# Kernel optimization log

Hardware: AMD Instinct MI355X
Metric: run time of the kernel (lower is better)

Reference implementation:

```python
import jax, jax.numpy as jnp
from jax import lax
import numpy as np

B, IMG, PS = 64, 384, 16
DM, DS, DI = 96, 16, 96
DT_RANK = 6
NREP = 4
NCLS = 5
HP = IMG // PS            # 24 patches per side
N = HP * HP               # 576 tokens


def _ln(x, g, b):
    m = x.mean(-1, keepdims=True)
    v = ((x - m) ** 2).mean(-1, keepdims=True)
    return (x - m) * lax.rsqrt(v + 1e-5) * g + b


def setup_inputs() -> dict:
    key = jax.random.key(0)
    ks = jax.random.split(key, 16)
    nrm = lambda k, s: jax.random.normal(k, s, jnp.float32) * 0.02
    return {
        "x": jax.random.uniform(ks[0], (B, 3, IMG, IMG), jnp.float32),
        "W_pe": nrm(ks[1], (DM, 3, PS, PS)), "b_pe": jnp.zeros((DM,), jnp.float32),
        "W_vis": nrm(ks[2], (DM, 1)), "b_vis": jnp.zeros((1,), jnp.float32),
        "dn_g": jnp.ones((DM,), jnp.float32), "dn_b": jnp.zeros((DM,), jnp.float32),
        "W_gate": nrm(ks[3], (DM, DM)), "b_gate": jnp.zeros((DM,), jnp.float32),
        "ln_g": jnp.ones((DM,), jnp.float32), "ln_b": jnp.zeros((DM,), jnp.float32),
        "W_in": nrm(ks[4], (DM, 2 * DI)),
        "conv_w": nrm(ks[5], (DI, 1, 3)),
        "W_xproj": nrm(ks[6], (DI, DT_RANK + 2 * DS)),
        "W_dt": nrm(ks[7], (DT_RANK, DI)), "b_dt": jnp.full((DI,), -2.0, jnp.float32),
        "A_log": jnp.log(jnp.tile(jnp.arange(1, DS + 1, dtype=jnp.float32), (DI, 1))),
        "D": jnp.ones((DI,), jnp.float32),
        "W_out": nrm(ks[8], (DI, DM)),
        "hd_dw": nrm(ks[9], (DM, 1, 3, 3)),
        "bn_g": jnp.ones((DM,), jnp.float32), "bn_b": jnp.zeros((DM,), jnp.float32),
        "bn_m": jnp.zeros((DM,), jnp.float32), "bn_v": jnp.ones((DM,), jnp.float32),
        "W_heat": nrm(ks[10], (NCLS, DM)), "b_heat": jnp.full((NCLS,), -2.19, jnp.float32),
        "W_off": nrm(ks[11], (2, DM)), "b_off": jnp.zeros((2,), jnp.float32),
        "W_size": nrm(ks[12], (2, DM)), "b_size": jnp.zeros((2,), jnp.float32),
    }


def _forward(x, W_pe, b_pe, W_vis, b_vis, dn_g, dn_b, W_gate, b_gate,
             ln_g, ln_b, W_in, conv_w, W_xproj, W_dt, b_dt, A_log, D, W_out,
             hd_dw, bn_g, bn_b, bn_m, bn_v, W_heat, b_heat, W_off, b_off, W_size, b_size):
    # --- retinex preprocessing (single-scale, log domain) ---
    kblur = jnp.ones((3, 1, 5, 5), jnp.float32) / 25.0
    L = lax.conv_general_dilated(x, kblur, (1, 1), 'SAME',
                                 feature_group_count=3,
                                 dimension_numbers=('NCHW', 'OIHW', 'NCHW'))
    x = jnp.log1p(jnp.clip(x, 0.0)) - jnp.log1p(jnp.clip(L, 0.0))
    # --- patch embedding: strided conv -> tokens (B,N,DM) ---
    t = lax.conv_general_dilated(x, W_pe, (PS, PS), 'VALID',
                                 dimension_numbers=('NCHW', 'OIHW', 'NCHW'))
    t = t + b_pe[None, :, None, None]
    tokens = t.reshape(B, DM, N).transpose(0, 2, 1)
    # --- visibility estimator: per-token gate (B,N,1) ---
    vis = jax.nn.sigmoid(tokens @ W_vis + b_vis)
    # --- dual norm: LN + sigmoid gate ---
    tokens = _ln(tokens, dn_g, dn_b)
    norm_gate = jax.nn.sigmoid(tokens @ W_gate + b_gate)  # (B,N,DM)
    # --- weight-shared NC-SSM blocks ---
    A = -jnp.exp(A_log)  # (DI,DS)
    for _ in range(NREP):
        resid = tokens
        h = _ln(tokens, ln_g, ln_b)
        xz = h @ W_in                      # (B,N,2*DI)
        xin, z = xz[..., :DI], xz[..., DI:]
        # causal depthwise conv1d over sequence, kernel 3
        xc = xin.transpose(0, 2, 1)        # (B,DI,N)
        xc = lax.conv_general_dilated(xc, conv_w, (1,), [(2, 0)],
                                      feature_group_count=DI,
                                      dimension_numbers=('NCH', 'OIH', 'NCH'))
        xs = jax.nn.silu(xc.transpose(0, 2, 1))  # (B,N,DI)
        # selective-scan parameters
        proj = xs @ W_xproj                # (B,N,DT_RANK+2*DS)
        dt_raw = proj[..., :DT_RANK]
        Bc = proj[..., DT_RANK:DT_RANK + DS]
        Cc = proj[..., DT_RANK + DS:]
        dt = jax.nn.softplus(dt_raw @ W_dt + b_dt)  # (B,N,DI)
        # time-major scan
        def step(hst, inp):
            dt_t, B_t, C_t, x_t = inp      # (B,DI),(B,DS),(B,DS),(B,DI)
            dA = jnp.exp(dt_t[:, :, None] * A)                 # (B,DI,DS)
            hst = dA * hst + (dt_t * x_t)[:, :, None] * B_t[:, None, :]
            y = jnp.einsum('bds,bs->bd', hst, C_t)
            return hst, y
        h0 = jnp.zeros((B, DI, DS), jnp.float32)
        _, ys = lax.scan(step, h0, (dt.transpose(1, 0, 2), Bc.transpose(1, 0, 2),
                                    Cc.transpose(1, 0, 2), xs.transpose(1, 0, 2)))
        y = ys.transpose(1, 0, 2) + D * xs           # (B,N,DI)
        y = y * jax.nn.silu(z) * vis                  # gated by z and visibility
        tokens = resid + (y @ W_out) * norm_gate
    # --- CenterNet-style head ---
    f = tokens.transpose(0, 2, 1).reshape(B, DM, HP, HP)
    g = lax.conv_general_dilated(f, hd_dw, (1, 1), 'SAME',
                                 feature_group_count=DM,
                                 dimension_numbers=('NCHW', 'OIHW', 'NCHW'))
    g = (g - bn_m[None, :, None, None]) * lax.rsqrt(bn_v + 1e-5)[None, :, None, None]
    g = jax.nn.silu(g * bn_g[None, :, None, None] + bn_b[None, :, None, None])
    heat = jnp.einsum('bchw,oc->bohw', g, W_heat) + b_heat[None, :, None, None]
    off = jnp.einsum('bchw,oc->bohw', f, W_off) + b_off[None, :, None, None]
    size = jnp.einsum('bchw,oc->bohw', f, W_size) + b_size[None, :, None, None]
    return heat, off, size


def reference(x, W_pe, b_pe, W_vis, b_vis, dn_g, dn_b, W_gate, b_gate,
              ln_g, ln_b, W_in, conv_w, W_xproj, W_dt, b_dt, A_log, D, W_out,
              hd_dw, bn_g, bn_b, bn_m, bn_v, W_heat, b_heat, W_off, b_off, W_size, b_size):
    return _forward(x, W_pe, b_pe, W_vis, b_vis, dn_g, dn_b, W_gate, b_gate,
                    ln_g, ln_b, W_in, conv_w, W_xproj, W_dt, b_dt, A_log, D, W_out,
                    hd_dw, bn_g, bn_b, bn_m, bn_v, W_heat, b_heat, W_off, b_off,
                    W_size, b_size)
```

## Files before the change

### kernel.cpp

```cpp
#include <hip/hip_runtime.h>

#define DEVINL __device__ __forceinline__

typedef __attribute__((ext_vector_type(8))) short bf8v;
typedef __attribute__((ext_vector_type(4))) float f4v;

DEVINL float b2f(unsigned short u){ union{unsigned int i; float f;} x; x.i = ((unsigned int)u)<<16; return x.f; }
DEVINL unsigned short f2b(float f){ union{float f; unsigned int i;} x; x.f = f; unsigned int r = x.i + 0x7FFFu + ((x.i>>16)&1u); return (unsigned short)(r>>16); }
DEVINL float sigf(float v){ return 1.f/(1.f + __expf(-v)); }
DEVINL void unpack8(const uint4 u, float* d){
  d[0]=b2f((unsigned short)(u.x)); d[1]=b2f((unsigned short)(u.x>>16));
  d[2]=b2f((unsigned short)(u.y)); d[3]=b2f((unsigned short)(u.y>>16));
  d[4]=b2f((unsigned short)(u.z)); d[5]=b2f((unsigned short)(u.z>>16));
  d[6]=b2f((unsigned short)(u.w)); d[7]=b2f((unsigned short)(u.w>>16));
}
DEVINL uint4 pack8(const float* s){
  uint4 u;
  u.x = (unsigned int)f2b(s[0]) | ((unsigned int)f2b(s[1])<<16);
  u.y = (unsigned int)f2b(s[2]) | ((unsigned int)f2b(s[3])<<16);
  u.z = (unsigned int)f2b(s[4]) | ((unsigned int)f2b(s[5])<<16);
  u.w = (unsigned int)f2b(s[6]) | ((unsigned int)f2b(s[7])<<16);
  return u;
}
union FragU { uint4 u; bf8v v; };


#define PREP_STRIDE (128*256)
__global__ __launch_bounds__(256) void k_prep(
    const float* __restrict__ Wgate, const float* __restrict__ Win,
    const float* __restrict__ Wxproj, const float* __restrict__ Wdt,
    const float* __restrict__ Wout, const float* __restrict__ Alog,
    const float* __restrict__ Wpe, const float* __restrict__ convw,
    unsigned short* __restrict__ WgT, unsigned short* __restrict__ WiT,
    unsigned short* __restrict__ WxT, unsigned short* __restrict__ WoT,
    float* __restrict__ Amat, unsigned short* __restrict__ WpeB,
    float* __restrict__ cwsplit)
{
  int gtid = blockIdx.x*256 + threadIdx.x;
  for (int i = gtid; i < 9216; i += PREP_STRIDE){
    int n = i/96, k = i - n*96;
    WgT[n*96+k] = f2b(Wgate[k*96+n]);
    WoT[n*96+k] = f2b(Wout[k*96+n]);
  }
  for (int i = gtid; i < 18432; i += PREP_STRIDE){
    int n = i/96, k = i - n*96;
    WiT[n*96+k] = f2b(Win[k*192+n]);
  }
  for (int i = gtid; i < 12288; i += PREP_STRIDE){
    int n = i/96, k = i - n*96;
    if (n < 96){
      float s = 0.f;
      for (int r = 0; r < 6; ++r) s += Wxproj[k*38+r] * Wdt[r*96+n];
      WxT[n*96+k] = f2b(s);
    } else {
      WxT[n*96+k] = f2b(Wxproj[k*38 + 6 + (n-96)]);
    }
  }
  for (int i = gtid; i < 1536; i += PREP_STRIDE) Amat[i] = -__expf(Alog[i]);
  for (int i = gtid; i < 73728; i += PREP_STRIDE) WpeB[i] = f2b(Wpe[i]);
  for (int i = gtid; i < 96; i += PREP_STRIDE){
    cwsplit[i]       = convw[i*3+0];
    cwsplit[96+i]    = convw[i*3+1];
    cwsplit[192+i]   = convw[i*3+2];
  }
}

__global__ __launch_bounds__(256) void k_blur(const float* __restrict__ x,
                                              unsigned short* __restrict__ xlog)
{
  __shared__ float xt[12*384];
  __shared__ float vt[8*392];
  int bid = blockIdx.x;
  int tile = bid % 48; int bc = bid / 48; int c = bc % 3; int b = bc / 3;
  const float* xin = x + (size_t)(b*3 + c) * 147456;
  unsigned short* xout = xlog + (size_t)(b*3 + c) * 147456;
  int y0 = tile * 8;
  int tid = threadIdx.x;

  #pragma unroll
  for (int k = 0; k < 5; ++k){
    int idx = tid + k*256;
    if (idx < 1152){
      int r = idx / 96; int c4 = idx - r*96;
      int gy = y0 - 2 + r;
      float4 v = make_float4(0.f,0.f,0.f,0.f);
      if (gy >= 0 && gy < 384) v = *(const float4*)(xin + gy*384 + c4*4);
      *(float4*)(xt + r*384 + c4*4) = v;
    }
  }
  if (tid < 64){
    int r = tid >> 3; int j = tid & 7;
    vt[r*392 + ((j < 4) ? j : (384 + j))] = 0.f;
  }
  __syncthreads();

  #pragma unroll
  for (int k = 0; k < 2; ++k){
    int cc = tid + k*256;
    if (cc < 384){
      float x0 = xt[cc], x1 = xt[384+cc], x2 = xt[768+cc],
            x3 = xt[1152+cc], x4 = xt[1536+cc];
      float vs = ((x0+x1)+(x2+x3))+x4;
      vt[4+cc] = vs;
      #pragma unroll
      for (int r = 1; r < 8; ++r){
        vs += xt[(r+4)*384+cc] - xt[(r-1)*384+cc];
        vt[r*392+4+cc] = vs;
      }
    }
  }
  __syncthreads();

  #pragma unroll
  for (int k = 0; k < 3; ++k){
    int unit = tid + k*256;
    int r = unit / 96; int c4 = unit - r*96;
    int base = r*392 + 4 + c4*4;
    float f[12];
    *(float4*)(f)   = *(const float4*)(vt + base - 4);
    *(float4*)(f+4) = *(const float4*)(vt + base);
    *(float4*)(f+8) = *(const float4*)(vt + base + 4);
    float xv[4];
    *(float4*)(xv) = *(const float4*)(xt + (r+2)*384 + c4*4);
    ushort4 o;
    unsigned short* op = &o.x;
    #pragma unroll
    for (int j = 0; j < 4; ++j){
      float s = f[2+j] + f[3+j] + f[4+j] + f[5+j] + f[6+j];
      float L = fmaxf(s * 0.04f, 0.f);
      float xc = fmaxf(xv[j], 0.f);
      op[j] = f2b(__logf(1.f + xc) - __logf(1.f + L));
    }
    *(ushort4*)(xout + (y0+r)*384 + c4*4) = o;
  }
}

__global__ __launch_bounds__(256) void k_patchln(
    const unsigned short* __restrict__ xlog, const unsigned short* __restrict__ WpeB,
    const float* __restrict__ bpe, const float* __restrict__ dng,
    const float* __restrict__ dnb, const float* __restrict__ Wvis,
    const float* __restrict__ bvis, float* __restrict__ tok, float* __restrict__ vis)
{
  int wid = threadIdx.x >> 6, lane = threadIdx.x & 63;
  int m0 = (blockIdx.x*4 + wid)*16;
  int l15 = lane & 15, q = lane >> 4;
  int ma0 = m0 + l15;
  int b0 = ma0/576; int r0 = ma0 - b0*576; int hp0 = r0/24; int wp0 = r0 - hp0*24;
  size_t base0 = (size_t)b0*442368 + (size_t)hp0*6144 + (size_t)wp0*16;
  f4v acc[6];
  #pragma unroll
  for (int j=0;j<6;++j)
    #pragma unroll
    for (int r=0;r<4;++r) acc[j][r] = 0.f;
  for (int ks = 0; ks < 24; ++ks){
    int k0 = ks*32 + q*8;
    int c  = k0 >> 8;
    int ph = (k0 >> 4) & 15;
    int pw = k0 & 15;
    size_t off = (size_t)c*147456 + (size_t)ph*384 + pw;
    bf8v a0 = *(const bf8v*)(xlog + base0 + off);
    #pragma unroll
    for (int nf = 0; nf < 6; ++nf){
      bf8v bb = *(const bf8v*)(WpeB + (size_t)(nf*16 + l15)*768 + k0);
      acc[nf] = __builtin_amdgcn_mfma_f32_16x16x32_bf16(a0, bb, acc[nf], 0, 0, 0);
    }
  }
  float v[6][4];
  float s[4], w[4], vd[4];
  #pragma unroll
  for (int r=0;r<4;++r){ s[r]=0.f; w[r]=0.f; vd[r]=0.f; }
  #pragma unroll
  for (int nf=0; nf<6; ++nf){
    int n = nf*16 + l15;
    float bp = bpe[n];
    float wv = Wvis[n];
    #pragma unroll
    for (int r=0;r<4;++r){
      float t = acc[nf][r] + bp;
      v[nf][r] = t;
      s[r] += t; w[r] += t*t; vd[r] += t*wv;
    }
  }
  #pragma unroll
  for (int off=1; off<16; off<<=1){
    #pragma unroll
    for (int r=0;r<4;++r){
      s[r]  += __shfl_xor(s[r],  off);
      w[r]  += __shfl_xor(w[r],  off);
      vd[r] += __shfl_xor(vd[r], off);
    }
  }
  float mu[4], rs[4];
  #pragma unroll
  for (int r=0;r<4;++r){
    mu[r] = s[r]*(1.f/96.f);
    rs[r] = rsqrtf(fmaxf(w[r]*(1.f/96.f)-mu[r]*mu[r], 0.f) + 1e-5f);
  }
  if (l15 == 0){
    #pragma unroll
    for (int r=0;r<4;++r) vis[m0 + q*4 + r] = sigf(vd[r] + bvis[0]);
  }
  #pragma unroll
  for (int nf=0; nf<6; ++nf){
    int n = nf*16 + l15;
    float g = dng[n], bb = dnb[n];
    #pragma unroll
    for (int r=0;r<4;++r)
      tok[(size_t)(m0 + q*4 + r)*96 + n] = (v[nf][r]-mu[r])*rs[r]*g + bb;
  }
}

__global__ __launch_bounds__(256) void k_lnfull(const float* __restrict__ tokp,
    const unsigned short* __restrict__ WgT, const float* __restrict__ bg,
    const float* __restrict__ lng, const float* __restrict__ lnb,
    const unsigned short* __restrict__ WiT, const float* __restrict__ vis,
    unsigned short* __restrict__ gate, unsigned short* __restrict__ xin,
    unsigned short* __restrict__ zsv)
{
  int wid = threadIdx.x >> 6, lane = threadIdx.x & 63;
  int gid = blockIdx.x*4 + wid;
  int tile = gid >> 1, half = gid & 1;
  int m0 = tile*16;
  int l15 = lane & 15, q = lane >> 4;
  int ma0 = m0 + l15;
  float a0v[24];
  float s1=0.f, w1=0.f;
  bf8v fa[3];
  #pragma unroll
  for (int ks = 0; ks < 3; ++ks){
    int k0 = ks*32 + q*8;
    float v0[8];
    #pragma unroll
    for (int h = 0; h < 2; ++h){
      float4 va = *(const float4*)(tokp + (size_t)ma0*96 + k0 + h*4);
      int o = ks*8 + h*4;
      a0v[o+0]=va.x; a0v[o+1]=va.y; a0v[o+2]=va.z; a0v[o+3]=va.w;
      v0[h*4+0]=va.x; v0[h*4+1]=va.y; v0[h*4+2]=va.z; v0[h*4+3]=va.w;
      s1 += (va.x+va.y)+(va.z+va.w);
      w1 += (va.x*va.x+va.y*va.y)+(va.z*va.z+va.w*va.w);
    }
    FragU U0; U0.u = pack8(v0);
    fa[ks] = U0.v;
  }
  s1 += __shfl_xor(s1, 16); s1 += __shfl_xor(s1, 32);
  w1 += __shfl_xor(w1, 16); w1 += __shfl_xor(w1, 32);
  float mu1 = s1*(1.f/96.f);
  float rs1 = rsqrtf(fmaxf(w1*(1.f/96.f)-mu1*mu1, 0.f) + 1e-5f);
  bf8v fb[3];
  #pragma unroll
  for (int ks = 0; ks < 3; ++ks){
    int k0 = ks*32 + q*8;
    float gv[8], bv[8];
    *(float4*)(gv)   = *(const float4*)(lng + k0);
    *(float4*)(gv+4) = *(const float4*)(lng + k0 + 4);
    *(float4*)(bv)   = *(const float4*)(lnb + k0);
    *(float4*)(bv+4) = *(const float4*)(lnb + k0 + 4);
    float v0[8];
    #pragma unroll
    for (int j = 0; j < 8; ++j)
      v0[j] = (a0v[ks*8+j]-mu1)*rs1*gv[j] + bv[j];
    FragU U0; U0.u = pack8(v0);
    fb[ks] = U0.v;
  }
  {
    f4v ag[3];
    #pragma unroll
    for (int j=0;j<3;++j)
      #pragma unroll
      for (int r=0;r<4;++r) ag[j][r] = 0.f;
    const bf8v* bpg = (const bf8v*)(WgT) + (size_t)l15*12 + q;
    #pragma unroll
    for (int ks = 0; ks < 3; ++ks)
      #pragma unroll
      for (int nf = 0; nf < 3; ++nf){
        bf8v bb = bpg[(half*3+nf)*192 + ks*4];
        ag[nf] = __builtin_amdgcn_mfma_f32_16x16x32_bf16(fa[ks], bb, ag[nf], 0, 0, 0);
      }
    #pragma unroll
    for (int nf=0; nf<3; ++nf)
      #pragma unroll
      for (int r=0; r<4; ++r){
        int m = m0 + q*4 + r;
        int n = (half*3+nf)*16 + l15;
        gate[(size_t)m*96 + n] = f2b(sigf(ag[nf][r] + bg[n]));
      }
  }
  {
    f4v aw[6];
    #pragma unroll
    for (int j=0;j<6;++j)
      #pragma unroll
      for (int r=0;r<4;++r) aw[j][r] = 0.f;
    const bf8v* bpw = (const bf8v*)(WiT) + (size_t)l15*12 + q;
    #pragma unroll
    for (int ks = 0; ks < 3; ++ks)
      #pragma unroll
      for (int nf = 0; nf < 6; ++nf){
        bf8v bb = bpw[(half*6+nf)*192 + ks*4];
        aw[nf] = __builtin_amdgcn_mfma_f32_16x16x32_bf16(fb[ks], bb, aw[nf], 0, 0, 0);
      }
    if (half == 0){
      #pragma unroll
      for (int nf=0; nf<6; ++nf)
        #pragma unroll
        for (int r=0; r<4; ++r){
          int m = m0 + q*4 + r;
          int n = nf*16 + l15;
          xin[(size_t)m*96 + n] = f2b(aw[nf][r]);
        }
    } else {
      #pragma unroll
      for (int nf=0; nf<6; ++nf)
        #pragma unroll
        for (int r=0; r<4; ++r){
          int m = m0 + q*4 + r;
          int n = nf*16 + l15;
          float v = aw[nf][r];
          float sgl = v * sigf(v);
          zsv[(size_t)m*96 + n] = f2b(sgl * vis[m]);
        }
    }
  }
}

__global__ __launch_bounds__(256) void k_patchfull(
    const unsigned short* __restrict__ xlog, const unsigned short* __restrict__ WpeB,
    const float* __restrict__ bpe,
    const float* __restrict__ dng, const float* __restrict__ dnb,
    const float* __restrict__ Wvis, const float* __restrict__ bvis,
    const unsigned short* __restrict__ WgT, const float* __restrict__ bg,
    const float* __restrict__ lng, const float* __restrict__ lnb,
    const unsigned short* __restrict__ WiT,
    float* __restrict__ tok, unsigned short* __restrict__ gate,
    float* __restrict__ vis, unsigned short* __restrict__ xin,
    unsigned short* __restrict__ zsv)
{
  __shared__ float Sl[2][16][100];
  __shared__ float Vl[2][16];
  int wid = threadIdx.x >> 6, lane = threadIdx.x & 63;
  int gid = blockIdx.x*4 + wid;
  int tile = gid >> 1, half = gid & 1;
  int tl = wid >> 1;
  int m0 = tile*16;
  int l15 = lane & 15, q = lane >> 4;
  int ma0 = m0 + l15;

  {
    int b0 = ma0/576; int r0 = ma0 - b0*576; int hp0 = r0/24; int wp0 = r0 - hp0*24;
    size_t base0 = (size_t)b0*442368 + (size_t)hp0*6144 + (size_t)wp0*16;
    f4v acc[3];
    #pragma unroll
    for (int j=0;j<3;++j)
      #pragma unroll
      for (int r=0;r<4;++r) acc[j][r] = 0.f;
    for (int ks = 0; ks < 24; ++ks){
      int k0 = ks*32 + q*8;
      int c  = k0 >> 8;
      int ph = (k0 >> 4) & 15;
      int pw = k0 & 15;
      size_t off = (size_t)c*147456 + (size_t)ph*384 + pw;
      bf8v a0 = *(const bf8v*)(xlog + base0 + off);
      #pragma unroll
      for (int nf = 0; nf < 3; ++nf){
        bf8v bb = *(const bf8v*)(WpeB + (size_t)((half*3+nf)*16 + l15)*768 + k0);
        acc[nf] = __builtin_amdgcn_mfma_f32_16x16x32_bf16(a0, bb, acc[nf], 0, 0, 0);
      }
    }
    #pragma unroll
    for (int nf=0; nf<3; ++nf)
      #pragma unroll
      for (int r=0; r<4; ++r){
        int n = (half*3+nf)*16 + l15;
        Sl[tl][q*4+r][n] = acc[nf][r] + bpe[n];
      }
  }
  __syncthreads();

  float a0v[24];
  float s0=0.f, w0=0.f, vd=0.f;
  #pragma unroll
  for (int ks = 0; ks < 3; ++ks){
    int k0 = ks*32 + q*8;
    #pragma unroll
    for (int h = 0; h < 2; ++h){
      float4 va = *(const float4*)(&Sl[tl][l15][k0 + h*4]);
      float4 wv = *(const float4*)(Wvis + k0 + h*4);
      int o = ks*8 + h*4;
      a0v[o+0]=va.x; a0v[o+1]=va.y; a0v[o+2]=va.z; a0v[o+3]=va.w;
      s0 += (va.x+va.y)+(va.z+va.w);
      w0 += (va.x*va.x+va.y*va.y)+(va.z*va.z+va.w*va.w);
      vd += (va.x*wv.x+va.y*wv.y)+(va.z*wv.z+va.w*wv.w);
    }
  }
  s0 += __shfl_xor(s0, 16); s0 += __shfl_xor(s0, 32);
  w0 += __shfl_xor(w0, 16); w0 += __shfl_xor(w0, 32);
  vd += __shfl_xor(vd, 16); vd += __shfl_xor(vd, 32);
  float mu0 = s0*(1.f/96.f);
  float rs0 = rsqrtf(fmaxf(w0*(1.f/96.f)-mu0*mu0, 0.f) + 1e-5f);
  if (half == 0 && q == 0){
    float vv = sigf(vd + bvis[0]);
    vis[ma0] = vv;
    Vl[tl][l15] = vv;
  }

  bf8v fa[3];
  float s1=0.f, w1=0.f;
  #pragma unroll
  for (int ks = 0; ks < 3; ++ks){
    int k0 = ks*32 + q*8;
    float gv[8], bv[8];
    *(float4*)(gv)   = *(const float4*)(dng + k0);
    *(float4*)(gv+4) = *(const float4*)(dng + k0 + 4);
    *(float4*)(bv)   = *(const float4*)(dnb + k0);
    *(float4*)(bv+4) = *(const float4*)(dnb + k0 + 4);
    float v0[8];
    #pragma unroll
    for (int j = 0; j < 8; ++j){
      float v = (a0v[ks*8+j]-mu0)*rs0*gv[j] + bv[j];
      v0[j] = v;
      a0v[ks*8+j] = v;
      s1 += v; w1 += v*v;
    }
    if (half == 0){
      *(float4*)(tok + (size_t)ma0*96 + k0)     = make_float4(v0[0],v0[1],v0[2],v0[3]);
      *(float4*)(tok + (size_t)ma0*96 + k0 + 4) = make_float4(v0[4],v0[5],v0[6],v0[7]);
    }
    FragU U0; U0.u = pack8(v0);
    fa[ks] = U0.v;
  }

  {
    f4v ag[3];
    #pragma unroll
    for (int j=0;j<3;++j)
      #pragma unroll
      for (int r=0;r<4;++r) ag[j][r] = 0.f;
    const bf8v* bpg = (const bf8v*)(WgT) + (size_t)l15*12 + q;
    #pragma unroll
    for (int ks = 0; ks < 3; ++ks)
      #pragma unroll
      for (int nf = 0; nf < 3; ++nf){
        bf8v bb = bpg[(half*3+nf)*192 + ks*4];
        ag[nf] = __builtin_amdgcn_mfma_f32_16x16x32_bf16(fa[ks], bb, ag[nf], 0, 0, 0);
      }
    #pragma unroll
    for (int nf=0; nf<3; ++nf)
      #pragma unroll
      for (int r=0; r<4; ++r){
        int m = m0 + q*4 + r;
        int n = (half*3+nf)*16 + l15;
        gate[(size_t)m*96 + n] = f2b(sigf(ag[nf][r] + bg[n]));
      }
  }

  s1 += __shfl_xor(s1, 16); s1 += __shfl_xor(s1, 32);
  w1 += __shfl_xor(w1, 16); w1 += __shfl_xor(w1, 32);
  float mu1 = s1*(1.f/96.f);
  float rs1 = rsqrtf(fmaxf(w1*(1.f/96.f)-mu1*mu1, 0.f) + 1e-5f);
  bf8v fb[3];
  #pragma unroll
  for (int ks = 0; ks < 3; ++ks){
    int k0 = ks*32 + q*8;
    float gv[8], bv[8];
    *(float4*)(gv)   = *(const float4*)(lng + k0);
    *(float4*)(gv+4) = *(const float4*)(lng + k0 + 4);
    *(float4*)(bv)   = *(const float4*)(lnb + k0);
    *(float4*)(bv+4) = *(const float4*)(lnb + k0 + 4);
    float v0[8];
    #pragma unroll
    for (int j = 0; j < 8; ++j)
      v0[j] = (a0v[ks*8+j]-mu1)*rs1*gv[j] + bv[j];
    FragU U0; U0.u = pack8(v0);
    fb[ks] = U0.v;
  }
  __syncthreads();

  {
    f4v aw[6];
    #pragma unroll
    for (int j=0;j<6;++j)
      #pragma unroll
      for (int r=0;r<4;++r) aw[j][r] = 0.f;
    const bf8v* bpw = (const bf8v*)(WiT) + (size_t)l15*12 + q;
    #pragma unroll
    for (int ks = 0; ks < 3; ++ks)
      #pragma unroll
      for (int nf = 0; nf < 6; ++nf){
        bf8v bb = bpw[(half*6+nf)*192 + ks*4];
        aw[nf] = __builtin_amdgcn_mfma_f32_16x16x32_bf16(fb[ks], bb, aw[nf], 0, 0, 0);
      }
    if (half == 0){
      #pragma unroll
      for (int nf=0; nf<6; ++nf)
        #pragma unroll
        for (int r=0; r<4; ++r){
          int m = m0 + q*4 + r;
          int n = nf*16 + l15;
          xin[(size_t)m*96 + n] = f2b(aw[nf][r]);
        }
    } else {
      #pragma unroll
      for (int nf=0; nf<6; ++nf)
        #pragma unroll
        for (int r=0; r<4; ++r){
          int m = m0 + q*4 + r;
          int n = nf*16 + l15;
          float v = aw[nf][r];
          float s = v * sigf(v);
          zsv[(size_t)m*96 + n] = f2b(s * Vl[tl][q*4+r]);
        }
    }
  }
}

template<bool DOLN>
__global__ __launch_bounds__(256) void k_woutln(
    const unsigned short* __restrict__ y2, const unsigned short* __restrict__ WoT,
    const unsigned short* __restrict__ gate,
    const float* __restrict__ lng, const float* __restrict__ lnb,
    const unsigned short* __restrict__ WiT, const float* __restrict__ vis,
    float* __restrict__ tok, unsigned short* __restrict__ xin,
    unsigned short* __restrict__ zsv)
{
  __shared__ float Sl[2][16][100];
  int wid = threadIdx.x >> 6, lane = threadIdx.x & 63;
  int gid = blockIdx.x*4 + wid;
  int tile = gid >> 1, half = gid & 1;
  int tl = wid >> 1;
  int m0 = tile*16;
  int l15 = lane & 15, q = lane >> 4;

  f4v acc[3];
  #pragma unroll
  for (int j=0;j<3;++j)
    #pragma unroll
    for (int r=0;r<4;++r) acc[j][r] = 0.f;
  const bf8v* a0p = (const bf8v*)(y2) + (size_t)(m0 + l15)*12 + q;
  const bf8v* bp  = (const bf8v*)(WoT) + (size_t)l15*12 + q;
  #pragma unroll
  for (int ks = 0; ks < 3; ++ks){
    bf8v a0 = a0p[ks*4];
    #pragma unroll
    for (int nf = 0; nf < 3; ++nf){
      bf8v bb = bp[(half*3+nf)*192 + ks*4];
      acc[nf] = __builtin_amdgcn_mfma_f32_16x16x32_bf16(a0, bb, acc[nf], 0, 0, 0);
    }
  }
  #pragma unroll
  for (int nf=0; nf<3; ++nf)
    #pragma unroll
    for (int r=0; r<4; ++r){
      int m = m0 + q*4 + r;
      int n = (half*3+nf)*16 + l15;
      size_t i = (size_t)m*96 + n;
      float tn = tok[i] + acc[nf][r] * b2f(gate[i]);
      tok[i] = tn;
      if constexpr (DOLN) Sl[tl][q*4+r][n] = tn;
    }

  if constexpr (DOLN){
    __syncthreads();
    int ma0 = m0 + l15;
    float a0v[24];
    float s0=0.f, w0=0.f;
    #pragma unroll
    for (int ks = 0; ks < 3; ++ks){
      int k0 = ks*32 + q*8;
      #pragma unroll
      for (int h = 0; h < 2; ++h){
        float4 va = *(const float4*)(&Sl[tl][l15][k0 + h*4]);
        int o = ks*8 + h*4;
        a0v[o+0]=va.x; a0v[o+1]=va.y; a0v[o+2]=va.z; a0v[o+3]=va.w;
        s0 += (va.x+va.y)+(va.z+va.w);
        w0 += (va.x*va.x+va.y*va.y)+(va.z*va.z+va.w*va.w);
      }
    }
    s0 += __shfl_xor(s0, 16); s0 += __shfl_xor(s0, 32);
    w0 += __shfl_xor(w0, 16); w0 += __shfl_xor(w0, 32);
    float mu0 = s0*(1.f/96.f);
    float rs0 = rsqrtf(fmaxf(w0*(1.f/96.f)-mu0*mu0, 0.f) + 1e-5f);
    bf8v fb[3];
    #pragma unroll
    for (int ks = 0; ks < 3; ++ks){
      int k0 = ks*32 + q*8;
      float gv[8], bv[8];
      *(float4*)(gv)   = *(const float4*)(lng + k0);
      *(float4*)(gv+4) = *(const float4*)(lng + k0 + 4);
      *(float4*)(bv)   = *(const float4*)(lnb + k0);
      *(float4*)(bv+4) = *(const float4*)(lnb + k0 + 4);
      float v0[8];
      #pragma unroll
      for (int j = 0; j < 8; ++j)
        v0[j] = (a0v[ks*8+j]-mu0)*rs0*gv[j] + bv[j];
      FragU U0; U0.u = pack8(v0);
      fb[ks] = U0.v;
    }
    f4v aw[6];
    #pragma unroll
    for (int j=0;j<6;++j)
      #pragma unroll
      for (int r=0;r<4;++r) aw[j][r] = 0.f;
    const bf8v* bpw = (const bf8v*)(WiT) + (size_t)l15*12 + q;
    #pragma unroll
    for (int ks = 0; ks < 3; ++ks)
      #pragma unroll
      for (int nf = 0; nf < 6; ++nf){
        bf8v bb = bpw[(half*6+nf)*192 + ks*4];
        aw[nf] = __builtin_amdgcn_mfma_f32_16x16x32_bf16(fb[ks], bb, aw[nf], 0, 0, 0);
      }
    if (half == 0){
      #pragma unroll
      for (int nf=0; nf<6; ++nf)
        #pragma unroll
        for (int r=0; r<4; ++r){
          int m = m0 + q*4 + r;
          int n = nf*16 + l15;
          xin[(size_t)m*96 + n] = f2b(aw[nf][r]);
        }
    } else {
      #pragma unroll
      for (int nf=0; nf<6; ++nf)
        #pragma unroll
        for (int r=0; r<4; ++r){
          int m = m0 + q*4 + r;
          int n = nf*16 + l15;
          float v = aw[nf][r];
          float sgl = v * sigf(v);
          zsv[(size_t)m*96 + n] = f2b(sgl * vis[m]);
        }
    }
  }
}

__global__ __launch_bounds__(256) void k_convxp(const unsigned short* __restrict__ xinb,
    const float* __restrict__ cwsplit, const unsigned short* __restrict__ BT,
    const float* __restrict__ bdt, unsigned short* __restrict__ xsb,
    unsigned short* __restrict__ dt, unsigned short* __restrict__ bc)
{
  int wid = threadIdx.x >> 6, lane = threadIdx.x & 63;
  int gid = blockIdx.x*4 + wid;
  int tile = gid >> 1, half = gid & 1;
  int m0 = tile*16;
  int nf0 = half*4;
  int l15 = lane & 15, q = lane >> 4;
  int ma0 = m0 + l15;
  int t0 = ma0 % 576;
  const float* cw0 = cwsplit;
  const float* cw1 = cwsplit + 96;
  const float* cw2 = cwsplit + 192;

  bf8v fa0[3];
  uint4 z4 = make_uint4(0,0,0,0);
  #pragma unroll
  for (int ks = 0; ks < 3; ++ks){
    int k0 = ks*32 + q*8;
    const unsigned short* r0p = xinb + (size_t)ma0*96 + k0;
    uint4 c0u  = *(const uint4*)(r0p);
    uint4 p10u = (t0 >= 1) ? *(const uint4*)(r0p - 96)  : z4;
    uint4 p20u = (t0 >= 2) ? *(const uint4*)(r0p - 192) : z4;
    float fc0[8], fp10[8], fp20[8];
    unpack8(c0u, fc0); unpack8(p10u, fp10); unpack8(p20u, fp20);
    float w0v[8], w1v[8], w2v[8];
    *(float4*)(w0v)   = *(const float4*)(cw0 + k0);
    *(float4*)(w0v+4) = *(const float4*)(cw0 + k0 + 4);
    *(float4*)(w1v)   = *(const float4*)(cw1 + k0);
    *(float4*)(w1v+4) = *(const float4*)(cw1 + k0 + 4);
    *(float4*)(w2v)   = *(const float4*)(cw2 + k0);
    *(float4*)(w2v+4) = *(const float4*)(cw2 + k0 + 4);
    float xs0[8];
    #pragma unroll
    for (int j = 0; j < 8; ++j){
      float v0 = w2v[j]*fc0[j] + w1v[j]*fp10[j] + w0v[j]*fp20[j];
      xs0[j] = v0 * sigf(v0);
    }
    FragU U0; U0.u = pack8(xs0);
    fa0[ks] = U0.v;
    if (half == 0) *(uint4*)(xsb + (size_t)ma0*96 + k0) = U0.u;
  }

  f4v acc[4];
  #pragma unroll
  for (int j=0;j<4;++j)
    #pragma unroll
    for (int r=0;r<4;++r) acc[j][r] = 0.f;
  const bf8v* bp = (const bf8v*)(BT) + (size_t)l15*12 + q;
  #pragma unroll
  for (int ks = 0; ks < 3; ++ks){
    #pragma unroll
    for (int nf = 0; nf < 4; ++nf){
      bf8v bb = bp[(nf0+nf)*192 + ks*4];
      acc[nf] = __builtin_amdgcn_mfma_f32_16x16x32_bf16(fa0[ks], bb, acc[nf], 0, 0, 0);
    }
  }
  #pragma unroll
  for (int nf=0; nf<4; ++nf)
    #pragma unroll
    for (int r=0; r<4; ++r){
      int m = m0 + q*4 + r;
      int n = (nf0+nf)*16 + l15;
      float v = acc[nf][r];
      if (n < 96){
        float xx = v + bdt[n];
        float sp = (xx > 20.f) ? xx : __logf(1.f + __expf(xx));
        dt[(size_t)m*96 + n] = f2b(sp);
      } else {
        bc[(size_t)m*32 + (n-96)] = f2b(v);
      }
    }
}

__global__ __launch_bounds__(512) void k_scan(const unsigned short* __restrict__ dt,
    const unsigned short* __restrict__ xsb, const unsigned short* __restrict__ bc,
    const unsigned short* __restrict__ zsv, const float* __restrict__ Amat,
    const float* __restrict__ Dw, unsigned short* __restrict__ y2)
{
  __shared__ float Ul[32*16*17];
  __shared__ float Sl[32*16];
  int b = blockIdx.x / 6; int dg = blockIdx.x - b*6;
  int tid = threadIdx.x;
  int c = tid >> 4; int dl = tid & 15; int d = dg*16 + dl;
  float As[16];
  #pragma unroll
  for (int s = 0; s < 16; s += 4){
    float4 t4 = *(const float4*)(Amat + d*16 + s);
    As[s]=t4.x; As[s+1]=t4.y; As[s+2]=t4.z; As[s+3]=t4.w;
  }
  bool fast = true;
  #pragma unroll
  for (int s = 0; s < 16; ++s)
    fast = fast && (fabsf(As[s] + (float)(s+1)) <= 2e-5f*(float)(s+1));

  float h[16];
  #pragma unroll
  for (int s=0;s<16;++s) h[s]=0.f;
  float sdt = 0.f;
  int tbase = b*576 + c*18;
  if (fast){
    for (int i = 0; i < 18; ++i){
      size_t m = (size_t)(tbase + i);
      float dtv = b2f(dt[m*96 + d]);
      float dtx = dtv * b2f(xsb[m*96 + d]);
      const uint4* bp = (const uint4*)(bc + m*32);
      float Bv[16];
      unpack8(bp[0], Bv); unpack8(bp[1], Bv+8);
      sdt += dtv;
      float w1=__expf(-dtv), w2=w1*w1, w3=w2*w1, w4=w2*w2;
      float w5=w4*w1, w6=w4*w2, w7=w4*w3, w8=w4*w4;
      float w9=w8*w1, w10=w8*w2, w11=w8*w3, w12=w8*w4;
      float w13=w8*w5, w14=w8*w6, w15=w8*w7, w16=w8*w8;
      float dA[16]={w1,w2,w3,w4,w5,w6,w7,w8,w9,w10,w11,w12,w13,w14,w15,w16};
      #pragma unroll
      for (int s=0;s<16;++s) h[s] = dA[s]*h[s] + dtx*Bv[s];
    }
  } else {
    for (int i = 0; i < 18; ++i){
      size_t m = (size_t)(tbase + i);
      float dtv = b2f(dt[m*96 + d]);
      float dtx = dtv * b2f(xsb[m*96 + d]);
      const uint4* bp = (const uint4*)(bc + m*32);
      float Bv[16];
      unpack8(bp[0], Bv); unpack8(bp[1], Bv+8);
      sdt += dtv;
      #pragma unroll
      for (int s=0;s<16;++s) h[s] = __expf(As[s]*dtv)*h[s] + dtx*Bv[s];
    }
  }
  {
    int base = (c*16 + dl)*17;
    #pragma unroll
    for (int s=0;s<16;++s) Ul[base + s] = h[s];
    Sl[c*16 + dl] = sdt;
  }
  __syncthreads();
  if (tid < 256){
    int dl2 = tid >> 4, s2 = tid & 15;
    float A2 = Amat[(dg*16 + dl2)*16 + s2];
    float hh = 0.f;
    for (int cc = 0; cc < 32; ++cc){
      float u = Ul[(cc*16 + dl2)*17 + s2];
      float ss = Sl[cc*16 + dl2];
      hh = __expf(A2*ss)*hh + u;
      Ul[(cc*16 + dl2)*17 + s2] = hh;
    }
  }
  __syncthreads();
  if (c == 0){
    #pragma unroll
    for (int s=0;s<16;++s) h[s] = 0.f;
  } else {
    int base = ((c-1)*16 + dl)*17;
    #pragma unroll
    for (int s=0;s<16;++s) h[s] = Ul[base + s];
  }
  float Dd = Dw[d];
  if (fast){
    for (int i = 0; i < 18; ++i){
      size_t m = (size_t)(tbase + i);
      float dtv = b2f(dt[m*96 + d]);
      float xv = b2f(xsb[m*96 + d]);
      float dtx = dtv * xv;
      const uint4* bp = (const uint4*)(bc + m*32);
      float Bv[16], Cv[16];
      unpack8(bp[0], Bv); unpack8(bp[1], Bv+8);
      unpack8(bp[2], Cv); unpack8(bp[3], Cv+8);
      float w1=__expf(-dtv), w2=w1*w1, w3=w2*w1, w4=w2*w2;
      float w5=w4*w1, w6=w4*w2, w7=w4*w3, w8=w4*w4;
      float w9=w8*w1, w10=w8*w2, w11=w8*w3, w12=w8*w4;
      float w13=w8*w5, w14=w8*w6, w15=w8*w7, w16=w8*w8;
      float dA[16]={w1,w2,w3,w4,w5,w6,w7,w8,w9,w10,w11,w12,w13,w14,w15,w16};
      float p0=0.f,p1=0.f,p2=0.f,p3=0.f;
      #pragma unroll
      for (int s=0;s<16;s+=4){
        h[s+0] = dA[s+0]*h[s+0] + dtx*Bv[s+0]; p0 += h[s+0]*Cv[s+0];
        h[s+1] = dA[s+1]*h[s+1] + dtx*Bv[s+1]; p1 += h[s+1]*Cv[s+1];
        h[s+2] = dA[s+2]*h[s+2] + dtx*Bv[s+2]; p2 += h[s+2]*Cv[s+2];
        h[s+3] = dA[s+3]*h[s+3] + dtx*Bv[s+3]; p3 += h[s+3]*Cv[s+3];
      }
      float y = (p0+p1) + (p2+p3);
      float yv = (y + Dd*xv) * b2f(zsv[m*96 + d]);
      y2[m*96 + d] = f2b(yv);
    }
  } else {
    for (int i = 0; i < 18; ++i){
      size_t m = (size_t)(tbase + i);
      float dtv = b2f(dt[m*96 + d]);
      float xv = b2f(xsb[m*96 + d]);
      float dtx = dtv * xv;
      const uint4* bp = (const uint4*)(bc + m*32);
      float Bv[16], Cv[16];
      unpack8(bp[0], Bv); unpack8(bp[1], Bv+8);
      unpack8(bp[2], Cv); unpack8(bp[3], Cv+8);
      float p0=0.f,p1=0.f,p2=0.f,p3=0.f;
      #pragma unroll
      for (int s=0;s<16;s+=4){
        h[s+0] = __expf(As[s+0]*dtv)*h[s+0] + dtx*Bv[s+0]; p0 += h[s+0]*Cv[s+0];
        h[s+1] = __expf(As[s+1]*dtv)*h[s+1] + dtx*Bv[s+1]; p1 += h[s+1]*Cv[s+1];
        h[s+2] = __expf(As[s+2]*dtv)*h[s+2] + dtx*Bv[s+2]; p2 += h[s+2]*Cv[s+2];
        h[s+3] = __expf(As[s+3]*dtv)*h[s+3] + dtx*Bv[s+3]; p3 += h[s+3]*Cv[s+3];
      }
      float y = (p0+p1) + (p2+p3);
      float yv = (y + Dd*xv) * b2f(zsv[m*96 + d]);
      y2[m*96 + d] = f2b(yv);
    }
  }
}

__global__ __launch_bounds__(256) void k_head(const float* __restrict__ tokens,
    const float* __restrict__ hdw, const float* __restrict__ bng,
    const float* __restrict__ bnb, const float* __restrict__ bnm,
    const float* __restrict__ bnv, const float* __restrict__ Wheat,
    const float* __restrict__ bheat, const float* __restrict__ Woff,
    const float* __restrict__ boff, const float* __restrict__ Wsize,
    const float* __restrict__ bsize, float* __restrict__ out)
{
  __shared__ float ft[3*2304];
  __shared__ float act[2304];
  int b = blockIdx.x / 24; int h = blockIdx.x - b*24;
  for (int i = threadIdx.x; i < 3*2304; i += 256){
    int rr = i / 2304; int j = i - rr*2304;
    int hh = h + rr - 1;
    float v = 0.f;
    if (hh >= 0 && hh < 24) v = tokens[((size_t)b*576 + hh*24)*96 + j];
    ft[rr*2304 + j] = v;
  }
  __syncthreads();
  for (int i = threadIdx.x; i < 2304; i += 256){
    int w = i / 96; int cc = i - w*96;
    float g = 0.f;
    #pragma unroll
    for (int dh = 0; dh < 3; ++dh){
      #pragma unroll
      for (int dw = 0; dw < 3; ++dw){
        int ww = w + dw - 1;
        if (ww >= 0 && ww < 24) g += ft[dh*2304 + ww*96 + cc] * hdw[cc*9 + dh*3 + dw];
      }
    }
    float gn = (g - bnm[cc]) * rsqrtf(bnv[cc] + 1e-5f);
    float a = gn * bng[cc] + bnb[cc];
    act[i] = a * sigf(a);
  }
  __syncthreads();
  int tid = threadIdx.x;
  if (tid < 120){
    int o = tid / 24; int w = tid - o*24;
    float s = 0.f;
    for (int cc = 0; cc < 96; ++cc) s += act[w*96 + cc] * Wheat[o*96 + cc];
    s += bheat[o];
    out[(size_t)b*2880 + o*576 + h*24 + w] = s;
  } else if (tid >= 128 && tid < 224){
    int idx = tid - 128; int o2 = idx / 24; int w = idx - o2*24;
    const float* W = (o2 < 2) ? Woff : Wsize;
    int o = o2 & 1;
    float s = 0.f;
    for (int cc = 0; cc < 96; ++cc) s += ft[2304 + w*96 + cc] * W[o*96 + cc];
    s += ((o2 < 2) ? boff : bsize)[o];
    size_t baseo = (o2 < 2) ? (size_t)184320 : (size_t)258048;
    out[baseo + (size_t)b*1152 + o*576 + h*24 + w] = s;
  }
}

extern "C" void kernel_launch(void* const* d_in, const int* in_sizes, int n_in,
                              void* d_out, int out_size, void* d_ws, size_t ws_size,
                              hipStream_t stream)
{
  (void)in_sizes; (void)n_in; (void)out_size;
  const float* x      = (const float*)d_in[0];
  const float* Wpe    = (const float*)d_in[1];
  const float* bpe    = (const float*)d_in[2];
  const float* Wvis   = (const float*)d_in[3];
  const float* bvis   = (const float*)d_in[4];
  const float* dng    = (const float*)d_in[5];
  const float* dnb    = (const float*)d_in[6];
  const float* Wgate  = (const float*)d_in[7];
  const float* bgate  = (const float*)d_in[8];
  const float* lng    = (const float*)d_in[9];
  const float* lnb    = (const float*)d_in[10];
  const float* Win    = (const float*)d_in[11];
  const float* convw  = (const float*)d_in[12];
  const float* Wxproj = (const float*)d_in[13];
  const float* Wdt    = (const float*)d_in[14];
  const float* bdt    = (const float*)d_in[15];
  const float* Alog   = (const float*)d_in[16];
  const float* Dw     = (const float*)d_in[17];
  const float* Wout   = (const float*)d_in[18];
  const float* hddw   = (const float*)d_in[19];
  const float* bng    = (const float*)d_in[20];
  const float* bnb    = (const float*)d_in[21];
  const float* bnm    = (const float*)d_in[22];
  const float* bnv    = (const float*)d_in[23];
  const float* Wheat  = (const float*)d_in[24];
  const float* bheat  = (const float*)d_in[25];
  const float* Woff   = (const float*)d_in[26];
  const float* boff   = (const float*)d_in[27];
  const float* Wsize  = (const float*)d_in[28];
  const float* bsize  = (const float*)d_in[29];
  float* out = (float*)d_out;

  const bool big = ws_size >= (size_t)120324096;
  char* ws = (char*)d_ws;

  size_t o_xlog = 0;
  size_t o_tok  = 56623104;
  size_t o_vis  = 70778880;
  size_t o_wgt  = 70926336;
  size_t o_wit  = 70944768;
  size_t o_wxt  = 70981632;
  size_t o_wot  = 71006208;
  size_t o_amat = 71024640;
  size_t o_wpe  = 71030784;
  size_t o_cw   = 71178240;
  size_t o_gate, o_xin, o_zsv, o_xsb, o_y2, o_dt, o_bc;
  if (big){
    o_gate = 75497472;  o_xin = 82575360;  o_zsv = 89653248;
    o_xsb  = 96731136;  o_y2  = 103809024; o_dt  = 110886912; o_bc = 117964800;
  } else {
    o_bc   = 0;         o_gate = 14155776; o_xsb = 21233664;
    o_y2   = 28311552;  o_xin  = 35389440; o_zsv = 42467328;  o_dt = 49545216;
  }

  unsigned short* xlog  = (unsigned short*)(ws + o_xlog);
  float*          tok   = (float*)(ws + o_tok);
  float*          vis   = (float*)(ws + o_vis);
  unsigned short* WgT   = (unsigned short*)(ws + o_wgt);
  unsigned short* WiT   = (unsigned short*)(ws + o_wit);
  unsigned short* WxT   = (unsigned short*)(ws + o_wxt);
  unsigned short* WoT   = (unsigned short*)(ws + o_wot);
  float*          Amat  = (float*)(ws + o_amat);
  unsigned short* WpeB  = (unsigned short*)(ws + o_wpe);
  float*          cwsp  = (float*)(ws + o_cw);
  unsigned short* gate  = (unsigned short*)(ws + o_gate);
  unsigned short* xinb  = (unsigned short*)(ws + o_xin);
  unsigned short* zsvb  = (unsigned short*)(ws + o_zsv);
  unsigned short* xsb   = (unsigned short*)(ws + o_xsb);
  unsigned short* y2    = (unsigned short*)(ws + o_y2);
  unsigned short* dtb   = (unsigned short*)(ws + o_dt);
  unsigned short* bcb   = (unsigned short*)(ws + o_bc);

  k_prep<<<128, 256, 0, stream>>>(Wgate, Win, Wxproj, Wdt, Wout, Alog, Wpe, convw,
                                  WgT, WiT, WxT, WoT, Amat, WpeB, cwsp);
  k_blur<<<9216, 256, 0, stream>>>(x, xlog);
  if (big){
    k_patchfull<<<1152, 256, 0, stream>>>(xlog, WpeB, bpe, dng, dnb, Wvis, bvis,
                                          WgT, bgate, lng, lnb, WiT,
                                          tok, gate, vis, xinb, zsvb);
  } else {
    k_patchln<<<576, 256, 0, stream>>>(xlog, WpeB, bpe, dng, dnb, Wvis, bvis, tok, vis);
    k_lnfull<<<1152, 256, 0, stream>>>(tok, WgT, bgate, lng, lnb, WiT, vis,
                                       gate, xinb, zsvb);
  }

  for (int rep = 0; rep < 4; ++rep){
    k_convxp<<<1152, 256, 0, stream>>>(xinb, cwsp, WxT, bdt, xsb, dtb, bcb);
    k_scan<<<384, 512, 0, stream>>>(dtb, xsb, bcb, zsvb, Amat, Dw, y2);
    if (rep < 3)
      k_woutln<true><<<1152, 256, 0, stream>>>(y2, WoT, gate, lng, lnb, WiT, vis,
                                               tok, xinb, zsvb);
    else
      k_woutln<false><<<1152, 256, 0, stream>>>(y2, WoT, gate, lng, lnb, WiT, vis,
                                                tok, xinb, zsvb);
  }

  k_head<<<1536, 256, 0, stream>>>(tok, hddw, bng, bnb, bnm, bnv,
                                   Wheat, bheat, Woff, boff, Wsize, bsize, out);
}
```

Measured before the change: 660.7 us.

## Transpose dt/xs for scan, move gating into Wout, bf16 blur tile

k_convxp now stages dt and xs in shared memory and writes them channel-major (per d, contiguous over time), so each k_scan thread loads its 16-step chunk with two vector loads instead of strided scalar reads. k_scan grows to 576 threads (36 chunks of 16 steps). The z-gate multiply moves from the scan into the Wout GEMM prologue, where y2 and zsv are multiplied before the MFMA. Separately, the blur kernel stores its input tile as bf16 and computes the vertical box sum directly for each row instead of as a running sum. That halves LDS use but rounds the input before the blur and the log, which may affect accuracy.

```diff
diff --git a/kernel.cpp b/kernel.cpp
--- a/kernel.cpp
+++ b/kernel.cpp
@@ -68,7 +68,7 @@
 __global__ __launch_bounds__(256) void k_blur(const float* __restrict__ x,
                                               unsigned short* __restrict__ xlog)
 {
-  __shared__ float xt[12*384];
+  __shared__ unsigned short xt[12*384];
   __shared__ float vt[8*392];
   int bid = blockIdx.x;
   int tile = bid % 48; int bc = bid / 48; int c = bc % 3; int b = bc / 3;
@@ -85,7 +85,8 @@
       int gy = y0 - 2 + r;
       float4 v = make_float4(0.f,0.f,0.f,0.f);
       if (gy >= 0 && gy < 384) v = *(const float4*)(xin + gy*384 + c4*4);
-      *(float4*)(xt + r*384 + c4*4) = v;
+      ushort4 o; o.x=f2b(v.x); o.y=f2b(v.y); o.z=f2b(v.z); o.w=f2b(v.w);
+      *(ushort4*)(xt + r*384 + c4*4) = o;
     }
   }
   if (tid < 64){
@@ -96,17 +97,23 @@
 
   #pragma unroll
   for (int k = 0; k < 2; ++k){
-    int cc = tid + k*256;
-    if (cc < 384){
-      float x0 = xt[cc], x1 = xt[384+cc], x2 = xt[768+cc],
-            x3 = xt[1152+cc], x4 = xt[1536+cc];
-      float vs = ((x0+x1)+(x2+x3))+x4;
-      vt[4+cc] = vs;
-      #pragma unroll
-      for (int r = 1; r < 8; ++r){
-        vs += xt[(r+4)*384+cc] - xt[(r-1)*384+cc];
-        vt[r*392+4+cc] = vs;
-      }
+    int unit = tid + k*256;
+    if (unit < 384){
+      int r = unit / 48; int c8 = unit - r*48;
+      const unsigned short* base = xt + r*384 + c8*8;
+      float acc[8]; float t[8];
+      uint4 u0 = *(const uint4*)(base);
+      unpack8(u0, acc);
+      #pragma unroll
+      for (int i = 1; i < 5; ++i){
+        uint4 u = *(const uint4*)(base + i*384);
+        unpack8(u, t);
+        #pragma unroll
+        for (int j = 0; j < 8; ++j) acc[j] += t[j];
+      }
+      float* vrow = vt + r*392 + 4 + c8*8;
+      *(float4*)(vrow)   = make_float4(acc[0],acc[1],acc[2],acc[3]);
+      *(float4*)(vrow+4) = make_float4(acc[4],acc[5],acc[6],acc[7]);
     }
   }
   __syncthreads();
@@ -120,16 +127,16 @@
     *(float4*)(f)   = *(const float4*)(vt + base - 4);
     *(float4*)(f+4) = *(const float4*)(vt + base);
     *(float4*)(f+8) = *(const float4*)(vt + base + 4);
-    float xv[4];
-    *(float4*)(xv) = *(const float4*)(xt + (r+2)*384 + c4*4);
+    ushort4 xr = *(const ushort4*)(xt + (r+2)*384 + c4*4);
+    const unsigned short* xrp = &xr.x;
     ushort4 o;
     unsigned short* op = &o.x;
     #pragma unroll
     for (int j = 0; j < 4; ++j){
       float s = f[2+j] + f[3+j] + f[4+j] + f[5+j] + f[6+j];
       float L = fmaxf(s * 0.04f, 0.f);
-      float xc = fmaxf(xv[j], 0.f);
-      op[j] = f2b(__logf(1.f + xc) - __logf(1.f + L));
+      float xv = fmaxf(b2f(xrp[j]), 0.f);
+      op[j] = f2b(__logf(1.f + xv) - __logf(1.f + L));
     }
     *(ushort4*)(xout + (y0+r)*384 + c4*4) = o;
   }
@@ -536,10 +543,18 @@
     #pragma unroll
     for (int r=0;r<4;++r) acc[j][r] = 0.f;
   const bf8v* a0p = (const bf8v*)(y2) + (size_t)(m0 + l15)*12 + q;
+  const bf8v* z0p = (const bf8v*)(zsv) + (size_t)(m0 + l15)*12 + q;
   const bf8v* bp  = (const bf8v*)(WoT) + (size_t)l15*12 + q;
   #pragma unroll
   for (int ks = 0; ks < 3; ++ks){
-    bf8v a0 = a0p[ks*4];
+    FragU Ua, Uz; Ua.v = a0p[ks*4]; Uz.v = z0p[ks*4];
+    float av[8], zv[8];
+    unpack8(Ua.u, av); unpack8(Uz.u, zv);
+    float pv[8];
+    #pragma unroll
+    for (int j = 0; j < 8; ++j) pv[j] = av[j]*zv[j];
+    FragU Up; Up.u = pack8(pv);
+    bf8v a0 = Up.v;
     #pragma unroll
     for (int nf = 0; nf < 3; ++nf){
       bf8v bb = bp[(half*3+nf)*192 + ks*4];
@@ -634,12 +649,15 @@
 
 __global__ __launch_bounds__(256) void k_convxp(const unsigned short* __restrict__ xinb,
     const float* __restrict__ cwsplit, const unsigned short* __restrict__ BT,
-    const float* __restrict__ bdt, unsigned short* __restrict__ xsb,
-    unsigned short* __restrict__ dt, unsigned short* __restrict__ bc)
+    const float* __restrict__ bdt, unsigned short* __restrict__ xs_t,
+    unsigned short* __restrict__ dt_t, unsigned short* __restrict__ bc)
 {
+  __shared__ unsigned short xs_l[2][96][16];
+  __shared__ unsigned short dt_l[2][96][16];
   int wid = threadIdx.x >> 6, lane = threadIdx.x & 63;
   int gid = blockIdx.x*4 + wid;
   int tile = gid >> 1, half = gid & 1;
+  int tl = wid >> 1;
   int m0 = tile*16;
   int nf0 = half*4;
   int l15 = lane & 15, q = lane >> 4;
@@ -675,7 +693,11 @@
     }
     FragU U0; U0.u = pack8(xs0);
     fa0[ks] = U0.v;
-    if (half == 0) *(uint4*)(xsb + (size_t)ma0*96 + k0) = U0.u;
+    if (half == 0){
+      const unsigned short* us = (const unsigned short*)&U0.u;
+      #pragma unroll
+      for (int j = 0; j < 8; ++j) xs_l[tl][k0+j][l15] = us[j];
+    }
   }
 
   f4v acc[4];
@@ -702,20 +724,34 @@
       if (n < 96){
         float xx = v + bdt[n];
         float sp = (xx > 20.f) ? xx : __logf(1.f + __expf(xx));
-        dt[(size_t)m*96 + n] = f2b(sp);
+        dt_l[tl][n][m - m0] = f2b(sp);
       } else {
         bc[(size_t)m*32 + (n-96)] = f2b(v);
       }
     }
-}
-
-__global__ __launch_bounds__(512) void k_scan(const unsigned short* __restrict__ dt,
-    const unsigned short* __restrict__ xsb, const unsigned short* __restrict__ bc,
-    const unsigned short* __restrict__ zsv, const float* __restrict__ Amat,
-    const float* __restrict__ Dw, unsigned short* __restrict__ y2)
+  __syncthreads();
+
+  for (int u = threadIdx.x; u < 384; u += 256){
+    int isdt = (u >= 192);
+    int v2 = isdt ? (u - 192) : u;
+    int tlo = v2 / 96; int k = v2 - tlo*96;
+    int mt = (blockIdx.x*2 + tlo)*16;
+    int b = mt / 576; int tloc = mt - b*576;
+    int row = (b*6 + (k >> 4))*16 + (k & 15);
+    const uint4* src = (const uint4*)(isdt ? &dt_l[tlo][k][0] : &xs_l[tlo][k][0]);
+    unsigned short* dst = (isdt ? dt_t : xs_t) + (size_t)row*576 + tloc;
+    ((uint4*)dst)[0] = src[0];
+    ((uint4*)dst)[1] = src[1];
+  }
+}
+
+__global__ __launch_bounds__(576) void k_scan(const unsigned short* __restrict__ dt_t,
+    const unsigned short* __restrict__ xs_t, const unsigned short* __restrict__ bc,
+    const float* __restrict__ Amat, const float* __restrict__ Dw,
+    unsigned short* __restrict__ y2)
 {
-  __shared__ float Ul[32*16*17];
-  __shared__ float Sl[32*16];
+  __shared__ float Ul[36*16*17];
+  __shared__ float Sl[36*16];
   int b = blockIdx.x / 6; int dg = blockIdx.x - b*6;
   int tid = threadIdx.x;
   int c = tid >> 4; int dl = tid & 15; int d = dg*16 + dl;
@@ -730,17 +766,25 @@
   for (int s = 0; s < 16; ++s)
     fast = fast && (fabsf(As[s] + (float)(s+1)) <= 2e-5f*(float)(s+1));
 
+  size_t rowoff = ((size_t)(b*6+dg)*16 + dl)*576 + (size_t)c*16;
+  const uint4* dtp = (const uint4*)(dt_t + rowoff);
+  const uint4* xsp = (const uint4*)(xs_t + rowoff);
+  uint4 du0 = dtp[0], du1 = dtp[1];
+  uint4 xu0 = xsp[0], xu1 = xsp[1];
+  float dts[16], xss[16];
+  unpack8(du0, dts); unpack8(du1, dts+8);
+  unpack8(xu0, xss); unpack8(xu1, xss+8);
+
   float h[16];
   #pragma unroll
   for (int s=0;s<16;++s) h[s]=0.f;
   float sdt = 0.f;
-  int tbase = b*576 + c*18;
+  size_t mbase = (size_t)b*576 + (size_t)c*16;
   if (fast){
-    for (int i = 0; i < 18; ++i){
-      size_t m = (size_t)(tbase + i);
-      float dtv = b2f(dt[m*96 + d]);
-      float dtx = dtv * b2f(xsb[m*96 + d]);
-      const uint4* bp = (const uint4*)(bc + m*32);
+    for (int i = 0; i < 16; ++i){
+      float dtv = dts[i];
+      float dtx = dtv * xss[i];
+      const uint4* bp = (const uint4*)(bc + (mbase+i)*32);
       float Bv[16];
       unpack8(bp[0], Bv); unpack8(bp[1], Bv+8);
       sdt += dtv;
@@ -753,11 +797,10 @@
       for (int s=0;s<16;++s) h[s] = dA[s]*h[s] + dtx*Bv[s];
     }
   } else {
-    for (int i = 0; i < 18; ++i){
-      size_t m = (size_t)(tbase + i);
-      float dtv = b2f(dt[m*96 + d]);
-      float dtx = dtv * b2f(xsb[m*96 + d]);
-      const uint4* bp = (const uint4*)(bc + m*32);
+    for (int i = 0; i < 16; ++i){
+      float dtv = dts[i];
+      float dtx = dtv * xss[i];
+      const uint4* bp = (const uint4*)(bc + (mbase+i)*32);
       float Bv[16];
       unpack8(bp[0], Bv); unpack8(bp[1], Bv+8);
       sdt += dtv;
@@ -776,7 +819,7 @@
     int dl2 = tid >> 4, s2 = tid & 15;
     float A2 = Amat[(dg*16 + dl2)*16 + s2];
     float hh = 0.f;
-    for (int cc = 0; cc < 32; ++cc){
+    for (int cc = 0; cc < 36; ++cc){
       float u = Ul[(cc*16 + dl2)*17 + s2];
       float ss = Sl[cc*16 + dl2];
       hh = __expf(A2*ss)*hh + u;
@@ -794,12 +837,11 @@
   }
   float Dd = Dw[d];
   if (fast){
-    for (int i = 0; i < 18; ++i){
-      size_t m = (size_t)(tbase + i);
-      float dtv = b2f(dt[m*96 + d]);
-      float xv = b2f(xsb[m*96 + d]);
+    for (int i = 0; i < 16; ++i){
+      float dtv = dts[i];
+      float xv = xss[i];
       float dtx = dtv * xv;
-      const uint4* bp = (const uint4*)(bc + m*32);
+      const uint4* bp = (const uint4*)(bc + (mbase+i)*32);
       float Bv[16], Cv[16];
       unpack8(bp[0], Bv); unpack8(bp[1], Bv+8);
       unpack8(bp[2], Cv); unpack8(bp[3], Cv+8);
@@ -817,16 +859,14 @@
         h[s+3] = dA[s+3]*h[s+3] + dtx*Bv[s+3]; p3 += h[s+3]*Cv[s+3];
       }
       float y = (p0+p1) + (p2+p3);
-      float yv = (y + Dd*xv) * b2f(zsv[m*96 + d]);
-      y2[m*96 + d] = f2b(yv);
+      y2[(mbase+i)*96 + d] = f2b(y + Dd*xv);
     }
   } else {
-    for (int i = 0; i < 18; ++i){
-      size_t m = (size_t)(tbase + i);
-      float dtv = b2f(dt[m*96 + d]);
-      float xv = b2f(xsb[m*96 + d]);
+    for (int i = 0; i < 16; ++i){
+      float dtv = dts[i];
+      float xv = xss[i];
       float dtx = dtv * xv;
-      const uint4* bp = (const uint4*)(bc + m*32);
+      const uint4* bp = (const uint4*)(bc + (mbase+i)*32);
       float Bv[16], Cv[16];
       unpack8(bp[0], Bv); unpack8(bp[1], Bv+8);
       unpack8(bp[2], Cv); unpack8(bp[3], Cv+8);
@@ -839,8 +879,7 @@
         h[s+3] = __expf(As[s+3]*dtv)*h[s+3] + dtx*Bv[s+3]; p3 += h[s+3]*Cv[s+3];
       }
       float y = (p0+p1) + (p2+p3);
-      float yv = (y + Dd*xv) * b2f(zsv[m*96 + d]);
-      y2[m*96 + d] = f2b(yv);
+      y2[(mbase+i)*96 + d] = f2b(y + Dd*xv);
     }
   }
 }
@@ -971,9 +1010,9 @@
   unsigned short* gate  = (unsigned short*)(ws + o_gate);
   unsigned short* xinb  = (unsigned short*)(ws + o_xin);
   unsigned short* zsvb  = (unsigned short*)(ws + o_zsv);
-  unsigned short* xsb   = (unsigned short*)(ws + o_xsb);
+  unsigned short* xst   = (unsigned short*)(ws + o_xsb);
   unsigned short* y2    = (unsigned short*)(ws + o_y2);
-  unsigned short* dtb   = (unsigned short*)(ws + o_dt);
+  unsigned short* dtt   = (unsigned short*)(ws + o_dt);
   unsigned short* bcb   = (unsigned short*)(ws + o_bc);
 
   k_prep<<<128, 256, 0, stream>>>(Wgate, Win, Wxproj, Wdt, Wout, Alog, Wpe, convw,
@@ -990,8 +1029,8 @@
   }
 
   for (int rep = 0; rep < 4; ++rep){
-    k_convxp<<<1152, 256, 0, stream>>>(xinb, cwsp, WxT, bdt, xsb, dtb, bcb);
-    k_scan<<<384, 512, 0, stream>>>(dtb, xsb, bcb, zsvb, Amat, Dw, y2);
+    k_convxp<<<1152, 256, 0, stream>>>(xinb, cwsp, WxT, bdt, xst, dtt, bcb);
+    k_scan<<<384, 576, 0, stream>>>(dtt, xst, bcb, Amat, Dw, y2);
     if (rep < 3)
       k_woutln<true><<<1152, 256, 0, stream>>>(y2, WoT, gate, lng, lnb, WiT, vis,
                                                tok, xinb, zsvb);
```

New measurement: 795.6 us. 20.4% more time.
